# Kernel tuning notes

Hardware: AMD Instinct MI355X
Metric: run time of the kernel (lower is better)

The kernel has to match this reference:

```python
import jax, jax.numpy as jnp
import numpy as np

M = 2          # n_mix
D_K = 128      # feature dim
TEMP = float(np.sqrt(D_K))  # temperature = d_k ** 0.5


def setup_inputs() -> dict:
    key = jax.random.key(0)
    k1, k2, k3, k4 = jax.random.split(key, 4)
    BS, N, N2 = 8, 2048, 2048
    qt = jax.random.normal(k1, (BS, N, D_K), jnp.float32)
    kt = jax.random.normal(k2, (BS, N2, D_K), jnp.float32)
    vt = jax.random.normal(k3, (BS, N2, D_K), jnp.float32)
    std = M ** -0.5
    kernel = jax.random.uniform(k4, (M, D_K), jnp.float32, -std, std)
    return {"qt": qt, "kt": kt, "vt": vt, "kernel": kernel}


def reference(qt, kt, vt, kernel):
    # channels_last path of MixtureOfSoftMaxACF.call, training=False (dropout = identity)
    BS, N, dk = qt.shape
    N2 = kt.shape[1]
    d = dk // M
    # mixture prior: softmax(kernel @ mean_q^T) over axis=1 (faithful to Softmax(axis=1))
    bar_qt = jnp.mean(qt, axis=1)                       # (BS, dk)
    prior_mix = jax.nn.softmax(kernel @ bar_qt.T, axis=1)  # (m, BS)
    prior_mix = prior_mix.reshape(BS * M, 1, 1)            # row-major reshape, as in TF
    # split features into mixtures via row-major reshape (as tf.reshape does)
    q = qt.reshape(BS * M, N, d)
    k = kt.reshape(BS * M, N2, d)
    att = jnp.einsum('bnd,bmd->bnm', q, k) / TEMP        # (BS*m, N, N2)
    att = jax.nn.softmax(att, axis=2)
    att = (att * prior_mix).reshape(BS, M, N, N2).sum(axis=1)  # (BS, N, N2)
    return att @ vt                                      # (BS, N, d_v)
```

## Files before the change

### kernel.cpp

```cpp
#include <hip/hip_runtime.h>
#include <hip/hip_fp16.h>

typedef float    f32x4 __attribute__((ext_vector_type(4)));
typedef _Float16 f16x2 __attribute__((ext_vector_type(2)));
typedef _Float16 f16x4 __attribute__((ext_vector_type(4)));
typedef _Float16 f16x8 __attribute__((ext_vector_type(8)));

#define BS 8
#define NN 2048
#define DK 128
#define DM 64
#define MIXOFF (1024 * DK)
#define QSCALE 0.12751744116926208f

#define MFMA32(a, b, c) __builtin_amdgcn_mfma_f32_16x16x32_f16((a), (b), (c), 0, 0, 0)
#define EXP2(x) __builtin_amdgcn_exp2f(x)

__device__ __forceinline__ f16x2 pkrtz(float x, float y) {
  return __builtin_bit_cast(f16x2, __builtin_amdgcn_cvt_pkrtz(x, y));
}

__device__ __forceinline__ void load_lds16(const _Float16* g, _Float16* l) {
  __builtin_amdgcn_global_load_lds(
      (const __attribute__((address_space(1))) void*)(uintptr_t)g,
      (__attribute__((address_space(3))) void*)(uint32_t)(uintptr_t)l, 16, 0, 0);
}

__global__ void prep_k(const float* __restrict__ kt, _Float16* __restrict__ kh,
                       const float* __restrict__ vt, _Float16* __restrict__ vT,
                       const float* __restrict__ qt, float* __restrict__ qpart) {
  __shared__ float tile[64][65];
  __shared__ float red[256];
  int blk = blockIdx.x;
  int t = threadIdx.x;
  if (blk < 512) {
    size_t base = (size_t)blk * 4096;
#pragma unroll
    for (int j = 0; j < 4; ++j) {
      size_t i = base + j * 1024 + t * 4;
      f32x4 v = *(const f32x4*)(kt + i);
      f16x4 h;
      h[0] = (_Float16)v[0]; h[1] = (_Float16)v[1];
      h[2] = (_Float16)v[2]; h[3] = (_Float16)v[3];
      *(f16x4*)(kh + i) = h;
    }
  } else if (blk < 1024) {
    int i2 = blk - 512;
    int b = i2 >> 6;
    int rem = i2 & 63;
    int j0 = (rem & 31) * 64;
    int c0 = (rem >> 5) * 64;
    int tx = t & 63, ty = t >> 6;
    const float* src = vt + ((size_t)b * NN + j0) * DK + c0;
#pragma unroll
    for (int rr = 0; rr < 16; ++rr) {
      int row = ty * 16 + rr;
      tile[row][tx] = src[(size_t)row * DK + tx];
    }
    __syncthreads();
    _Float16* dst = vT + ((size_t)b * DK + c0) * NN + j0;
    int chl = t >> 4;
    int k4 = (t & 15) * 4;
#pragma unroll
    for (int r2 = 0; r2 < 4; ++r2) {
      int ch = r2 * 16 + chl;
      f16x4 h;
      h[0] = (_Float16)tile[k4 + 0][ch]; h[1] = (_Float16)tile[k4 + 1][ch];
      h[2] = (_Float16)tile[k4 + 2][ch]; h[3] = (_Float16)tile[k4 + 3][ch];
      *(f16x4*)(dst + (size_t)ch * NN + k4) = h;
    }
  } else {
    int i = blk - 1024;
    int b = i >> 3, seg = i & 7;
    int c = t & 127, h = t >> 7;
    const float* p = qt + ((size_t)b * NN + seg * 256 + h * 128) * DK + c;
    float s = 0.f;
#pragma unroll 8
    for (int n = 0; n < 128; ++n) s += p[(size_t)n * DK];
    red[t] = s;
    __syncthreads();
    if (t < 128) qpart[(size_t)i * 128 + t] = red[t] + red[t + 128];
  }
}

#define STAGE(BUF, S) do {                                                  \
    _Float16* db_ = stg + (BUF) * 16384;                                    \
    load_lds16(khg + gKst + (S) * 4096,        db_ + t * 8);                \
    load_lds16(khg + gKst + (S) * 4096 + 2048, db_ + 4096 + t * 8);         \
    load_lds16(vTg + gVst + (S) * 64,          db_ + 8192 + t * 8);         \
    load_lds16(vTg + gVst + (S) * 64 + 32,     db_ + 12288 + t * 8);        \
  } while (0)

__global__ __launch_bounds__(512, 2) void attn_k(const float* __restrict__ qt,
                                                 const _Float16* __restrict__ khg,
                                                 const _Float16* __restrict__ vTg,
                                                 float* __restrict__ opart,
                                                 float* __restrict__ lpart) {
  __shared__ __align__(16) char smem[65536];
  _Float16* stg = (_Float16*)smem;
  const int b = blockIdx.x & 7;
  const int qb = (blockIdx.x >> 3) & 15;
  const int kb = blockIdx.x >> 7;
  const int t = threadIdx.x;
  const int wv = t >> 6;
  const int m = wv >> 2;
  const int u = wv & 3;
  const int lane = t & 63;
  const int quad = lane >> 4, l16 = lane & 15;
  const int perm = ((l16 >> 2) << 3) | (l16 & 3);
  const int bq = b * (NN * DK);
  const int bV = b * (DK * NN);

  f16x8 qf[2][2];
#pragma unroll
  for (int su = 0; su < 2; ++su)
#pragma unroll
    for (int c = 0; c < 2; ++c) {
      const float* qp_ = qt + bq + m * MIXOFF +
                         (qb * 128 + u * 32 + su * 16 + l16) * DM + quad * 8 + c * 32;
      f32x4 v0 = *(const f32x4*)qp_;
      f32x4 v1 = *(const f32x4*)(qp_ + 4);
      union { f16x8 v; f16x2 h[4]; } w;
      w.h[0] = pkrtz(v0[0] * QSCALE, v0[1] * QSCALE);
      w.h[1] = pkrtz(v0[2] * QSCALE, v0[3] * QSCALE);
      w.h[2] = pkrtz(v1[0] * QSCALE, v1[1] * QSCALE);
      w.h[3] = pkrtz(v1[2] * QSCALE, v1[3] * QSCALE);
      qf[su][c] = w.v;
    }

  const int mixu = t >> 8;
  const int qq8 = t & 255;
  const int rK = qq8 >> 3;
  const int uuK = (qq8 & 7) ^ ((rK & 3) ^ (((rK >> 3) & 1) << 2));
  const int chV = t >> 2;
  const int uuV = (t & 3) ^ ((chV + (chV >> 2)) & 3);
  const int gKst = bq + mixu * MIXOFF + kb * 65536 + rK * 64 + uuK * 8;
  const int gVst = bV + chV * NN + kb * 1024 + uuV * 8;

  const int gK = (l16 & 3) ^ (((l16 >> 2) & 1) << 2);
  const int hV = (l16 + (l16 >> 2)) & 3;
  const int kA = (quad ^ gK) * 8;
  const int kB = ((quad + 4) ^ gK) * 8;
  const int kbase = m * 2048 + perm * 64;
  const int vboff = l16 * 32 + (quad ^ hV) * 8;

  const f32x4 z = {0.f, 0.f, 0.f, 0.f};
  f32x4 acc[2][8];
  float lsum[2] = {0.f, 0.f};
#pragma unroll
  for (int su = 0; su < 2; ++su)
#pragma unroll
    for (int cc = 0; cc < 8; ++cc) acc[su][cc] = z;

  STAGE(0, 0);
  int buf = 0;
  for (int s = 0; s < 16; ++s) {
    __syncthreads();
    if (s + 1 < 16) STAGE(buf ^ 1, s + 1);
    const _Float16* sb_ = stg + buf * 16384;
#pragma unroll
    for (int hh = 0; hh < 2; ++hh) {
      const _Float16* kp_ = sb_ + hh * 4096 + kbase;
      f16x8 kf0 = *(const f16x8*)(kp_ + kA);
      f16x8 kf1 = *(const f16x8*)(kp_ + kB);
      f16x8 kf2 = *(const f16x8*)(kp_ + 256 + kA);
      f16x8 kf3 = *(const f16x8*)(kp_ + 256 + kB);
      f16x8 pw[2];
#pragma unroll
      for (int su = 0; su < 2; ++su) {
        f32x4 s0 = MFMA32(kf1, qf[su][1], MFMA32(kf0, qf[su][0], z));
        f32x4 s1 = MFMA32(kf3, qf[su][1], MFMA32(kf2, qf[su][0], z));
        float e0 = EXP2(s0[0]), e1 = EXP2(s0[1]), e2 = EXP2(s0[2]), e3 = EXP2(s0[3]);
        float e4 = EXP2(s1[0]), e5 = EXP2(s1[1]), e6 = EXP2(s1[2]), e7 = EXP2(s1[3]);
        lsum[su] += ((e0 + e1) + (e2 + e3)) + ((e4 + e5) + (e6 + e7));
        union { f16x8 v; f16x2 h[4]; } w;
        w.h[0] = pkrtz(e0, e1); w.h[1] = pkrtz(e2, e3);
        w.h[2] = pkrtz(e4, e5); w.h[3] = pkrtz(e6, e7);
        pw[su] = w.v;
      }
      const _Float16* vb_ = sb_ + 8192 + hh * 4096 + vboff;
      f16x8 vf[8];
#pragma unroll
      for (int cc = 0; cc < 8; ++cc) vf[cc] = *(const f16x8*)(vb_ + cc * 512);
#pragma unroll
      for (int cc = 0; cc < 8; ++cc)
#pragma unroll
        for (int su = 0; su < 2; ++su) acc[su][cc] = MFMA32(vf[cc], pw[su], acc[su][cc]);
    }
    buf ^= 1;
  }

#pragma unroll
  for (int su = 0; su < 2; ++su) {
    lsum[su] += __shfl_xor(lsum[su], 16);
    lsum[su] += __shfl_xor(lsum[su], 32);
  }
  const size_t plane = (size_t)((b * 2 + kb) * 2 + m);
#pragma unroll
  for (int su = 0; su < 2; ++su) {
    const int qg = qb * 128 + u * 32 + su * 16 + l16;
    if (quad == 0) lpart[plane * 2048 + qg] = lsum[su];
    float* op = opart + (plane * 2048 + qg) * (size_t)128 + quad * 4;
#pragma unroll
    for (int cc = 0; cc < 8; ++cc) *(f32x4*)(op + cc * 16) = acc[su][cc];
  }
}

__global__ __launch_bounds__(256) void merge_k(const float* __restrict__ qpart,
                                               const float* __restrict__ kern,
                                               const float* __restrict__ opart,
                                               const float* __restrict__ lpart,
                                               float* __restrict__ out) {
  __shared__ float barL[1024];
  __shared__ float lgp[16], exq[16], prp[16];
  const int t = threadIdx.x;
  const int b = blockIdx.x & 7;
  const int qc = blockIdx.x >> 3;
  for (int e = t; e < 1024; e += 256) {
    int bb = e >> 7, c = e & 127;
    float ss = 0.f;
#pragma unroll
    for (int seg = 0; seg < 8; ++seg) ss += qpart[(size_t)(bb * 8 + seg) * 128 + c];
    barL[e] = ss * (1.0f / 2048.0f);
  }
  __syncthreads();
  if (t < 16) {
    int mm = t >> 3, bb = t & 7;
    float ss = 0.f;
    for (int c = 0; c < DK; ++c) ss += kern[mm * DK + c] * barL[bb * 128 + c];
    lgp[t] = ss;
  }
  __syncthreads();
  if (t < 16) {
    int mm = t >> 3;
    float mx = lgp[mm * 8];
    for (int i2 = 1; i2 < 8; ++i2) mx = fmaxf(mx, lgp[mm * 8 + i2]);
    exq[t] = __expf(lgp[t] - mx);
  }
  __syncthreads();
  if (t < 16) {
    int mm = t >> 3;
    float sm = 0.f;
    for (int i2 = 0; i2 < 8; ++i2) sm += exq[mm * 8 + i2];
    prp[t] = exq[t] / sm;
  }
  __syncthreads();
  const float w0 = prp[b * 2 + 0], w1 = prp[b * 2 + 1];
  const int q = qc * 64 + (t >> 2);
  const int dc = (t & 3) * 32;
  const float l00 = lpart[((b * 2 + 0) * 2 + 0) * 2048 + q];
  const float l01 = lpart[((b * 2 + 0) * 2 + 1) * 2048 + q];
  const float l10 = lpart[((b * 2 + 1) * 2 + 0) * 2048 + q];
  const float l11 = lpart[((b * 2 + 1) * 2 + 1) * 2048 + q];
  const float r0 = w0 / (l00 + l10);
  const float r1 = w1 / (l01 + l11);
  const float* p00 = opart + ((size_t)(((b * 2 + 0) * 2 + 0) * 2048 + q)) * 128 + dc;
  const float* p01 = opart + ((size_t)(((b * 2 + 0) * 2 + 1) * 2048 + q)) * 128 + dc;
  const float* p10 = opart + ((size_t)(((b * 2 + 1) * 2 + 0) * 2048 + q)) * 128 + dc;
  const float* p11 = opart + ((size_t)(((b * 2 + 1) * 2 + 1) * 2048 + q)) * 128 + dc;
  float* po = out + ((size_t)b * NN + q) * DK + dc;
#pragma unroll
  for (int g = 0; g < 8; ++g) {
    f32x4 a0 = *(const f32x4*)(p00 + g * 4);
    f32x4 a1 = *(const f32x4*)(p01 + g * 4);
    f32x4 b0 = *(const f32x4*)(p10 + g * 4);
    f32x4 b1 = *(const f32x4*)(p11 + g * 4);
    f32x4 o;
#pragma unroll
    for (int e = 0; e < 4; ++e) o[e] = (a0[e] + b0[e]) * r0 + (a1[e] + b1[e]) * r1;
    *(f32x4*)(po + g * 4) = o;
  }
}

extern "C" void kernel_launch(void* const* d_in, const int* in_sizes, int n_in,
                              void* d_out, int out_size, void* d_ws, size_t ws_size,
                              hipStream_t stream) {
  const float* qt = (const float*)d_in[0];
  const float* kt = (const float*)d_in[1];
  const float* vt = (const float*)d_in[2];
  const float* kern = (const float*)d_in[3];
  float* out = (float*)d_out;

  char* ws = (char*)d_ws;
  float* qpart = (float*)(ws + 4096);
  _Float16* khp = (_Float16*)(ws + 65536);
  _Float16* vTp = khp + (size_t)BS * NN * DK;
  float* opart = (float*)(ws + (16u << 20));
  float* lpart = (float*)(ws + (48u << 20));

  prep_k<<<dim3(1088), dim3(256), 0, stream>>>(kt, khp, vt, vTp, qt, qpart);
  attn_k<<<dim3(256), dim3(512), 0, stream>>>(qt, khp, vTp, opart, lpart);
  merge_k<<<dim3(256), dim3(256), 0, stream>>>(qpart, kern, opart, lpart, out);
}
```

Before: 131.6 us.

## Split attention into more smaller blocks with four-way key split

Rework the attention kernel to run 1024 blocks of 256 threads instead of 256 blocks of 512. Each block now covers 64 query rows and a quarter of the keys, with half-size LDS staging per step. The merge kernel reduces four key-split partials instead of two. This aims to fill all CUs with more resident blocks, but it doubles the partial output written to and read from global memory and enlarges the workspace.

```diff
diff --git a/kernel.cpp b/kernel.cpp
--- a/kernel.cpp
+++ b/kernel.cpp
@@ -84,27 +84,27 @@
 }
 
 #define STAGE(BUF, S) do {                                                  \
-    _Float16* db_ = stg + (BUF) * 16384;                                    \
-    load_lds16(khg + gKst + (S) * 4096,        db_ + t * 8);                \
-    load_lds16(khg + gKst + (S) * 4096 + 2048, db_ + 4096 + t * 8);         \
-    load_lds16(vTg + gVst + (S) * 64,          db_ + 8192 + t * 8);         \
-    load_lds16(vTg + gVst + (S) * 64 + 32,     db_ + 12288 + t * 8);        \
+    _Float16* db_ = stg + (BUF) * 8192;                                     \
+    load_lds16(khg + gKst + (S) * 2048,          db_ + t * 8);              \
+    load_lds16(khg + gKst + MIXOFF + (S) * 2048, db_ + 2048 + t * 8);       \
+    load_lds16(vTg + gVst + (S) * 32,            db_ + 4096 + t * 8);       \
+    load_lds16(vTg + gVst + 64 * NN + (S) * 32,  db_ + 6144 + t * 8);       \
   } while (0)
 
-__global__ __launch_bounds__(512, 2) void attn_k(const float* __restrict__ qt,
+__global__ __launch_bounds__(256, 4) void attn_k(const float* __restrict__ qt,
                                                  const _Float16* __restrict__ khg,
                                                  const _Float16* __restrict__ vTg,
                                                  float* __restrict__ opart,
                                                  float* __restrict__ lpart) {
-  __shared__ __align__(16) char smem[65536];
+  __shared__ __align__(16) char smem[32768];
   _Float16* stg = (_Float16*)smem;
   const int b = blockIdx.x & 7;
-  const int qb = (blockIdx.x >> 3) & 15;
-  const int kb = blockIdx.x >> 7;
+  const int qb = (blockIdx.x >> 3) & 31;
+  const int kb = blockIdx.x >> 8;
   const int t = threadIdx.x;
   const int wv = t >> 6;
-  const int m = wv >> 2;
-  const int u = wv & 3;
+  const int m = wv >> 1;
+  const int u = wv & 1;
   const int lane = t & 63;
   const int quad = lane >> 4, l16 = lane & 15;
   const int perm = ((l16 >> 2) << 3) | (l16 & 3);
@@ -117,7 +117,7 @@
 #pragma unroll
     for (int c = 0; c < 2; ++c) {
       const float* qp_ = qt + bq + m * MIXOFF +
-                         (qb * 128 + u * 32 + su * 16 + l16) * DM + quad * 8 + c * 32;
+                         (qb * 64 + u * 32 + su * 16 + l16) * DM + quad * 8 + c * 32;
       f32x4 v0 = *(const f32x4*)qp_;
       f32x4 v1 = *(const f32x4*)(qp_ + 4);
       union { f16x8 v; f16x2 h[4]; } w;
@@ -128,21 +128,19 @@
       qf[su][c] = w.v;
     }
 
-  const int mixu = t >> 8;
-  const int qq8 = t & 255;
-  const int rK = qq8 >> 3;
-  const int uuK = (qq8 & 7) ^ ((rK & 3) ^ (((rK >> 3) & 1) << 2));
+  const int rK = t >> 3;
+  const int uuK = (t & 7) ^ ((rK & 3) ^ (((rK >> 3) & 1) << 2));
   const int chV = t >> 2;
   const int uuV = (t & 3) ^ ((chV + (chV >> 2)) & 3);
-  const int gKst = bq + mixu * MIXOFF + kb * 65536 + rK * 64 + uuK * 8;
-  const int gVst = bV + chV * NN + kb * 1024 + uuV * 8;
+  const int gKst = bq + kb * 32768 + rK * 64 + uuK * 8;
+  const int gVst = bV + chV * NN + kb * 512 + uuV * 8;
 
   const int gK = (l16 & 3) ^ (((l16 >> 2) & 1) << 2);
   const int hV = (l16 + (l16 >> 2)) & 3;
   const int kA = (quad ^ gK) * 8;
   const int kB = ((quad + 4) ^ gK) * 8;
   const int kbase = m * 2048 + perm * 64;
-  const int vboff = l16 * 32 + (quad ^ hV) * 8;
+  const int vboff = 4096 + l16 * 32 + (quad ^ hV) * 8;
 
   const f32x4 z = {0.f, 0.f, 0.f, 0.f};
   f32x4 acc[2][8];
@@ -157,36 +155,33 @@
   for (int s = 0; s < 16; ++s) {
     __syncthreads();
     if (s + 1 < 16) STAGE(buf ^ 1, s + 1);
-    const _Float16* sb_ = stg + buf * 16384;
-#pragma unroll
-    for (int hh = 0; hh < 2; ++hh) {
-      const _Float16* kp_ = sb_ + hh * 4096 + kbase;
-      f16x8 kf0 = *(const f16x8*)(kp_ + kA);
-      f16x8 kf1 = *(const f16x8*)(kp_ + kB);
-      f16x8 kf2 = *(const f16x8*)(kp_ + 256 + kA);
-      f16x8 kf3 = *(const f16x8*)(kp_ + 256 + kB);
-      f16x8 pw[2];
-#pragma unroll
-      for (int su = 0; su < 2; ++su) {
-        f32x4 s0 = MFMA32(kf1, qf[su][1], MFMA32(kf0, qf[su][0], z));
-        f32x4 s1 = MFMA32(kf3, qf[su][1], MFMA32(kf2, qf[su][0], z));
-        float e0 = EXP2(s0[0]), e1 = EXP2(s0[1]), e2 = EXP2(s0[2]), e3 = EXP2(s0[3]);
-        float e4 = EXP2(s1[0]), e5 = EXP2(s1[1]), e6 = EXP2(s1[2]), e7 = EXP2(s1[3]);
-        lsum[su] += ((e0 + e1) + (e2 + e3)) + ((e4 + e5) + (e6 + e7));
-        union { f16x8 v; f16x2 h[4]; } w;
-        w.h[0] = pkrtz(e0, e1); w.h[1] = pkrtz(e2, e3);
-        w.h[2] = pkrtz(e4, e5); w.h[3] = pkrtz(e6, e7);
-        pw[su] = w.v;
-      }
-      const _Float16* vb_ = sb_ + 8192 + hh * 4096 + vboff;
-      f16x8 vf[8];
-#pragma unroll
-      for (int cc = 0; cc < 8; ++cc) vf[cc] = *(const f16x8*)(vb_ + cc * 512);
-#pragma unroll
-      for (int cc = 0; cc < 8; ++cc)
-#pragma unroll
-        for (int su = 0; su < 2; ++su) acc[su][cc] = MFMA32(vf[cc], pw[su], acc[su][cc]);
-    }
+    const _Float16* sb_ = stg + buf * 8192;
+    const _Float16* kp_ = sb_ + kbase;
+    f16x8 kf0 = *(const f16x8*)(kp_ + kA);
+    f16x8 kf1 = *(const f16x8*)(kp_ + kB);
+    f16x8 kf2 = *(const f16x8*)(kp_ + 256 + kA);
+    f16x8 kf3 = *(const f16x8*)(kp_ + 256 + kB);
+    f16x8 pw[2];
+#pragma unroll
+    for (int su = 0; su < 2; ++su) {
+      f32x4 s0 = MFMA32(kf1, qf[su][1], MFMA32(kf0, qf[su][0], z));
+      f32x4 s1 = MFMA32(kf3, qf[su][1], MFMA32(kf2, qf[su][0], z));
+      float e0 = EXP2(s0[0]), e1 = EXP2(s0[1]), e2 = EXP2(s0[2]), e3 = EXP2(s0[3]);
+      float e4 = EXP2(s1[0]), e5 = EXP2(s1[1]), e6 = EXP2(s1[2]), e7 = EXP2(s1[3]);
+      lsum[su] += ((e0 + e1) + (e2 + e3)) + ((e4 + e5) + (e6 + e7));
+      union { f16x8 v; f16x2 h[4]; } w;
+      w.h[0] = pkrtz(e0, e1); w.h[1] = pkrtz(e2, e3);
+      w.h[2] = pkrtz(e4, e5); w.h[3] = pkrtz(e6, e7);
+      pw[su] = w.v;
+    }
+    const _Float16* vb_ = sb_ + vboff;
+    f16x8 vf[8];
+#pragma unroll
+    for (int cc = 0; cc < 8; ++cc) vf[cc] = *(const f16x8*)(vb_ + cc * 512);
+#pragma unroll
+    for (int cc = 0; cc < 8; ++cc)
+#pragma unroll
+      for (int su = 0; su < 2; ++su) acc[su][cc] = MFMA32(vf[cc], pw[su], acc[su][cc]);
     buf ^= 1;
   }
 
@@ -195,10 +190,10 @@
     lsum[su] += __shfl_xor(lsum[su], 16);
     lsum[su] += __shfl_xor(lsum[su], 32);
   }
-  const size_t plane = (size_t)((b * 2 + kb) * 2 + m);
+  const size_t plane = (size_t)((b * 4 + kb) * 2 + m);
 #pragma unroll
   for (int su = 0; su < 2; ++su) {
-    const int qg = qb * 128 + u * 32 + su * 16 + l16;
+    const int qg = qb * 64 + u * 32 + su * 16 + l16;
     if (quad == 0) lpart[plane * 2048 + qg] = lsum[su];
     float* op = opart + (plane * 2048 + qg) * (size_t)128 + quad * 4;
 #pragma unroll
@@ -248,26 +243,27 @@
   const float w0 = prp[b * 2 + 0], w1 = prp[b * 2 + 1];
   const int q = qc * 64 + (t >> 2);
   const int dc = (t & 3) * 32;
-  const float l00 = lpart[((b * 2 + 0) * 2 + 0) * 2048 + q];
-  const float l01 = lpart[((b * 2 + 0) * 2 + 1) * 2048 + q];
-  const float l10 = lpart[((b * 2 + 1) * 2 + 0) * 2048 + q];
-  const float l11 = lpart[((b * 2 + 1) * 2 + 1) * 2048 + q];
-  const float r0 = w0 / (l00 + l10);
-  const float r1 = w1 / (l01 + l11);
-  const float* p00 = opart + ((size_t)(((b * 2 + 0) * 2 + 0) * 2048 + q)) * 128 + dc;
-  const float* p01 = opart + ((size_t)(((b * 2 + 0) * 2 + 1) * 2048 + q)) * 128 + dc;
-  const float* p10 = opart + ((size_t)(((b * 2 + 1) * 2 + 0) * 2048 + q)) * 128 + dc;
-  const float* p11 = opart + ((size_t)(((b * 2 + 1) * 2 + 1) * 2048 + q)) * 128 + dc;
+  float l0 = 0.f, l1 = 0.f;
+#pragma unroll
+  for (int kb = 0; kb < 4; ++kb) {
+    l0 += lpart[((size_t)((b * 4 + kb) * 2 + 0)) * 2048 + q];
+    l1 += lpart[((size_t)((b * 4 + kb) * 2 + 1)) * 2048 + q];
+  }
+  const float r0 = w0 / l0;
+  const float r1 = w1 / l1;
   float* po = out + ((size_t)b * NN + q) * DK + dc;
 #pragma unroll
   for (int g = 0; g < 8; ++g) {
-    f32x4 a0 = *(const f32x4*)(p00 + g * 4);
-    f32x4 a1 = *(const f32x4*)(p01 + g * 4);
-    f32x4 b0 = *(const f32x4*)(p10 + g * 4);
-    f32x4 b1 = *(const f32x4*)(p11 + g * 4);
-    f32x4 o;
-#pragma unroll
-    for (int e = 0; e < 4; ++e) o[e] = (a0[e] + b0[e]) * r0 + (a1[e] + b1[e]) * r1;
+    f32x4 o = {0.f, 0.f, 0.f, 0.f};
+#pragma unroll
+    for (int kb = 0; kb < 4; ++kb) {
+      const float* p0 = opart + (((size_t)((b * 4 + kb) * 2 + 0)) * 2048 + q) * 128 + dc;
+      const float* p1 = opart + (((size_t)((b * 4 + kb) * 2 + 1)) * 2048 + q) * 128 + dc;
+      f32x4 a0 = *(const f32x4*)(p0 + g * 4);
+      f32x4 a1 = *(const f32x4*)(p1 + g * 4);
+#pragma unroll
+      for (int e = 0; e < 4; ++e) o[e] += a0[e] * r0 + a1[e] * r1;
+    }
     *(f32x4*)(po + g * 4) = o;
   }
 }
@@ -285,10 +281,10 @@
   float* qpart = (float*)(ws + 4096);
   _Float16* khp = (_Float16*)(ws + 65536);
   _Float16* vTp = khp + (size_t)BS * NN * DK;
-  float* opart = (float*)(ws + (16u << 20));
-  float* lpart = (float*)(ws + (48u << 20));
+  float* opart = (float*)(ws + (32u << 20));
+  float* lpart = (float*)(ws + (96u << 20));
 
   prep_k<<<dim3(1088), dim3(256), 0, stream>>>(kt, khp, vt, vTp, qt, qpart);
-  attn_k<<<dim3(256), dim3(512), 0, stream>>>(qt, khp, vTp, opart, lpart);
+  attn_k<<<dim3(1024), dim3(256), 0, stream>>>(qt, khp, vTp, opart, lpart);
   merge_k<<<dim3(256), dim3(256), 0, stream>>>(qpart, kern, opart, lpart, out);
 }
```

Result: slower. 195.6 us (+48.7%).
